# Performance work log

Measured on AMD Instinct MI355X. Metric: run time of the kernel, lower is better.

Reference implementation:

```python
import jax, jax.numpy as jnp
import numpy as np


def _conv2d(x, w, b):
    # NCHW valid conv, kernel shape OIHW
    y = jax.lax.conv_general_dilated(x, w, (1, 1), 'VALID',
                                     dimension_numbers=('NCHW', 'OIHW', 'NCHW'))
    return y + b[None, :, None, None]


def _rgcn(x, src, dst, edge_type, root, rel, bias):
    # PyG RGCNConv: out_i = x_i @ root + bias + sum_r mean_{j in N_r(i)} x_j @ W_r
    # x: [B, N, F]; src/dst: [E]; rel: [R, F, F]
    out = x @ root + bias
    N = x.shape[1]
    for r in range(rel.shape[0]):  # small fixed relation count
        m = (edge_type == r).astype(x.dtype)                # [E]
        msg = (x @ rel[r])[:, src] * m[None, :, None]       # [B, E, F]
        agg = jnp.zeros_like(out).at[:, dst].add(msg)       # [B, N, F]
        cnt = jnp.zeros((N,), x.dtype).at[dst].add(m)       # per-node relation degree
        out = out + agg / jnp.clip(cnt, 1.0)[None, :, None]
    return out


def setup_inputs() -> dict:
    key = jax.random.key(0)
    ks = jax.random.split(key, 16)
    B, C, N, T = 16, 3, 3000, 50
    E, R, S, F = 96000, 3, 500, 43  # F = 2*20 + 3
    observation = jax.random.normal(ks[0], (B, C, N, T), jnp.float32)
    last_action = jax.random.uniform(ks[1], (B, S + 1), dtype=jnp.float32)
    edge_index = jax.random.randint(ks[2], (2, E), 0, N, jnp.int32)
    edge_type = jax.random.randint(ks[3], (E,), 0, R, jnp.int32)
    nodes_to_select = jnp.sort(jax.random.randint(ks[4], (S,), 0, N, jnp.int32))

    def w(k, shape, fan_in):
        return jax.random.normal(k, shape, jnp.float32) / np.sqrt(fan_in).astype(np.float32)

    params = dict(
        ws1=w(ks[5], (3, 3, 1, 3), 9), bs1=jnp.zeros(3, jnp.float32),
        ws2=w(ks[6], (20, 3, 1, 48), 144), bs2=jnp.zeros(20, jnp.float32),
        wm1=w(ks[7], (3, 3, 1, 21), 63), bm1=jnp.zeros(3, jnp.float32),
        wm2=w(ks[8], (20, 3, 1, 30), 90), bm2=jnp.zeros(20, jnp.float32),
        root1=w(ks[9], (F, F), F), rel1=w(ks[10], (R, F, F), F), bias1=jnp.zeros(F, jnp.float32),
        root2=w(ks[11], (F, F), F), rel2=w(ks[12], (R, F, F), F), bias2=jnp.zeros(F, jnp.float32),
        wf=w(ks[13], (1, 87, 1, 1), 87), bf=jnp.zeros(1, jnp.float32),
    )
    return {"observation": observation, "last_action": last_action,
            "edge_index": edge_index, "edge_type": edge_type,
            "nodes_to_select": nodes_to_select, **params}


def reference(observation, last_action, edge_index, edge_type, nodes_to_select,
              ws1, bs1, ws2, bs2, wm1, bm1, wm2, bm2,
              root1, rel1, bias1, root2, rel2, bias2, wf, bf):
    relu = jax.nn.relu
    B = observation.shape[0]
    last_stocks = last_action[:, 1:][:, None, :, None]                      # [B,1,S,1]
    short = relu(_conv2d(relu(_conv2d(observation, ws1, bs1)), ws2, bs2))   # [B,20,N,1]
    mid = relu(_conv2d(relu(_conv2d(observation, wm1, bm1)), wm2, bm2))     # [B,20,N,1]
    longf = relu(jnp.max(observation, axis=3, keepdims=True))               # [B,3,N,1]
    temporal = jnp.concatenate([short, mid, longf], axis=1)                 # [B,43,N,1]
    x = jnp.transpose(temporal[..., 0], (0, 2, 1))                          # [B,N,43]
    src, dst = edge_index[0], edge_index[1]
    h = jax.nn.leaky_relu(_rgcn(x, src, dst, edge_type, root1, rel1, bias1), 0.01)
    h = jax.nn.leaky_relu(_rgcn(h, src, dst, edge_type, root2, rel2, bias2), 0.01)
    graph_features = jnp.transpose(h, (0, 2, 1))[..., None]                 # [B,43,N,1]
    feats = jnp.concatenate([temporal, graph_features], axis=1)             # [B,86,N,1]
    feats = feats[:, :, nodes_to_select, :]                                 # [B,86,S,1]
    feats = jnp.concatenate([last_stocks, feats], axis=1)                   # [B,87,S,1]
    out = _conv2d(feats, wf, bf)                                            # [B,1,S,1]
    cash = jnp.zeros((B, 1, 1, 1), out.dtype)  # cash bias zeroed in mu()
    logits = jnp.concatenate([cash, out], axis=2)[:, 0, :, 0]               # [B,S+1]
    return jax.nn.softmax(logits, axis=-1)  # softmax_temperature = 1
```

## Files before the change

kernel.cpp:

```cpp
#include <hip/hip_runtime.h>
#include <math.h>

#define NB 16
#define NC 3
#define NN 3000
#define NT 50
#define NE 96000
#define NR 3
#define NS 500
#define NF 43
#define NFP 44
#define NBF (NB*NFP)
#define NBKT (NR*NN)
#define CAP 96
#define PREF 24

#define XT_OFF   0
#define H1_OFF   (XT_OFF + NN*NBF)
#define LG_OFF   (H1_OFF + NN*NBF)
#define INT_BASE (LG_OFF + NB*(NS+1))
#define CNT_OFF  0
#define EBUF_OFF (CNT_OFF + NBKT)

#define TS 51

__global__ __launch_bounds__(256, 3) void k_front(
    const float* __restrict__ obs,
    const float* __restrict__ ws1, const float* __restrict__ bs1,
    const float* __restrict__ ws2, const float* __restrict__ bs2,
    const float* __restrict__ wm1, const float* __restrict__ bm1,
    const float* __restrict__ wm2, const float* __restrict__ bm2,
    float* __restrict__ x,
    const int* __restrict__ ei, const int* __restrict__ et,
    int* __restrict__ cnt, int* __restrict__ ebuf)
{
    __shared__ float smem[3 * 64 * TS];
    int tid = threadIdx.x;

    if (blockIdx.x >= 1500) {
        int e = (blockIdx.x - 1500) * 256 + tid;
        int bkt = et[e] * NN + ei[NE + e];
        int pos = atomicAdd(&cnt[bkt], 1);
        if (pos < CAP) ebuf[bkt * CAP + pos] = ei[e];
        return;
    }

    int wave = __builtin_amdgcn_readfirstlane(tid >> 6);
    int lane = tid & 63;
    bool isA = blockIdx.x < 750;
    int idx0 = (isA ? blockIdx.x : blockIdx.x - 750) * 64;

    #pragma unroll
    for (int k = 0; k < 19; ++k) {
        int f2 = k * 256 + tid;
        if (f2 < 4800) {
            int c = f2 / 1600;
            int rem = f2 - c * 1600;
            int nr = rem / 25;
            int tp = rem - nr * 25;
            int idx = idx0 + nr;
            int b = idx / NN, n = idx - b * NN;
            float2 u = *(const float2*)(obs + ((size_t)(b * NC + c) * NN + n) * NT + 2 * tp);
            float* d = &smem[(c * 64 + nr) * TS + 2 * tp];
            d[0] = u.x; d[1] = u.y;
        }
    }
    __syncthreads();

    #define SP(w, nd, o) smem[((w) * 64 + (nd)) * 23 + (o)]

    if (isA) {
        int base = 12 * wave;
        float wS[3][14];
        #pragma unroll
        for (int c = 0; c < 3; ++c) {
            const float* sr = &smem[(c * 64 + lane) * TS + base];
            #pragma unroll
            for (int jj = 0; jj < 14; ++jj) wS[c][jj] = sr[jj];
        }
        __syncthreads();

        float acc[20];
        #pragma unroll
        for (int o = 0; o < 20; ++o) acc[o] = 0.f;
        #pragma unroll
        for (int j = 0; j < 12; ++j) {
            float y[3];
            #pragma unroll
            for (int c = 0; c < 3; ++c) {
                float s = bs1[c];
                #pragma unroll
                for (int i = 0; i < 3; ++i)
                    #pragma unroll
                    for (int k = 0; k < 3; ++k)
                        s = fmaf(wS[i][j + k], ws1[(c * 3 + i) * 3 + k], s);
                y[c] = fmaxf(s, 0.f);
            }
            int gt = base + j;
            #pragma unroll
            for (int o = 0; o < 20; ++o) {
                float a = acc[o];
                #pragma unroll
                for (int c = 0; c < 3; ++c)
                    a = fmaf(y[c], ws2[(o * 3 + c) * 48 + gt], a);
                acc[o] = a;
            }
        }
        #pragma unroll
        for (int o = 0; o < 20; ++o) SP(wave, lane, o) = acc[o];
        __syncthreads();
        #pragma unroll
        for (int q = 0; q < 5; ++q) {
            int item = q * 256 + tid;
            int node = item / 20, o = item - node * 20;
            int g = idx0 + node;
            int bb = g / NN, nn = g - bb * NN;
            float s = ((SP(0, node, o) + SP(1, node, o)) +
                       (SP(2, node, o) + SP(3, node, o))) + bs2[o];
            x[(size_t)nn * NBF + bb * NFP + o] = fmaxf(s, 0.f);
        }
        return;
    }

    {
        int mbase = (wave < 3) ? 8 * wave : 24;
        int nld   = (wave < 3) ? 28 : 26;

        float s[3][8];
        #pragma unroll
        for (int c = 0; c < 3; ++c)
            #pragma unroll
            for (int t = 0; t < 8; ++t) s[c][t] = bm1[c];
        float cmax[3];
        float wA[28], wB[28];

        #define LOADW(buf, ch)                                              \
        {                                                                   \
            const float* sr = &smem[((ch) * 64 + lane) * TS + mbase];       \
            _Pragma("unroll")                                               \
            for (int t = 0; t < 28; ++t)                                    \
                buf[t] = (t < nld) ? sr[t] : 0.f;                           \
        }
        #define COMPW(buf, ii)                                              \
        {                                                                   \
            float m = buf[0];                                               \
            _Pragma("unroll")                                               \
            for (int t = 1; t < 28; ++t) m = fmaxf(m, buf[t]);              \
            cmax[ii] = m;                                                   \
            _Pragma("unroll")                                               \
            for (int c = 0; c < 3; ++c)                                     \
                _Pragma("unroll")                                           \
                for (int t = 0; t < 8; ++t) {                               \
                    float a = s[c][t];                                      \
                    _Pragma("unroll")                                       \
                    for (int k = 0; k < 21; ++k)                            \
                        a = fmaf(buf[t + k], wm1[(c * 3 + (ii)) * 21 + k], a); \
                    s[c][t] = a;                                            \
                }                                                           \
        }

        LOADW(wA, 0)
        LOADW(wB, 1)
        COMPW(wA, 0)
        LOADW(wA, 2)
        COMPW(wB, 1)
        COMPW(wA, 2)
        #undef LOADW
        #undef COMPW
        __syncthreads();

        float acc[20];
        #pragma unroll
        for (int o = 0; o < 20; ++o) acc[o] = 0.f;
        int cntM = (wave < 3) ? 8 : 6;
        #pragma unroll
        for (int j = 0; j < 8; ++j) {
            if (j < cntM) {
                float y0 = fmaxf(s[0][j], 0.f);
                float y1 = fmaxf(s[1][j], 0.f);
                float y2 = fmaxf(s[2][j], 0.f);
                int gt = mbase + j;
                #pragma unroll
                for (int o = 0; o < 20; ++o) {
                    float a = acc[o];
                    a = fmaf(y0, wm2[(o * 3 + 0) * 30 + gt], a);
                    a = fmaf(y1, wm2[(o * 3 + 1) * 30 + gt], a);
                    a = fmaf(y2, wm2[(o * 3 + 2) * 30 + gt], a);
                    acc[o] = a;
                }
            }
        }
        #pragma unroll
        for (int o = 0; o < 20; ++o) SP(wave, lane, o) = acc[o];
        #pragma unroll
        for (int c = 0; c < 3; ++c) SP(wave, lane, 20 + c) = cmax[c];
    }
    __syncthreads();
    #pragma unroll
    for (int q = 0; q < 6; ++q) {
        int item = q * 256 + tid;
        if (item < 1472) {
            int node = item / 23, o = item - node * 23;
            int g = idx0 + node;
            int bb = g / NN, nn = g - bb * NN;
            size_t row = (size_t)nn * NBF + bb * NFP;
            if (o < 20) {
                float s = ((SP(0, node, o) + SP(1, node, o)) +
                           (SP(2, node, o) + SP(3, node, o))) + bm2[o];
                x[row + 20 + o] = fmaxf(s, 0.f);
            } else {
                float m = fmaxf(fmaxf(SP(0, node, o), SP(1, node, o)),
                                fmaxf(SP(2, node, o), SP(3, node, o)));
                x[row + 40 + (o - 20)] = fmaxf(m, 0.f);
            }
        }
    }
    #undef SP
}

template<bool LEAKY, bool SEL>
__global__ __launch_bounds__(256) void k_rgcn(
    const float* __restrict__ in, const float* __restrict__ xsrc,
    const int* __restrict__ cnt, const int* __restrict__ ebuf,
    const int* __restrict__ sel,
    const float* __restrict__ root, const float* __restrict__ rel,
    const float* __restrict__ bias,
    const float* __restrict__ la, const float* __restrict__ wf,
    const float* __restrict__ bf,
    float* __restrict__ out)
{
    __shared__ __align__(16) float lrow[4][NBF];
    __shared__ float sP[8][4][NFP];

    int tid = threadIdx.x;
    int wave = __builtin_amdgcn_readfirstlane(tid >> 6);
    int lane = tid & 63;
    int i = blockIdx.x;
    int node = __builtin_amdgcn_readfirstlane(SEL ? sel[i] : i);

    const float* wbase = (wave == 0) ? root : (rel + (size_t)(wave - 1) * NF * NF);
    float wsl[43];
    #pragma unroll
    for (int j = 0; j < 43; ++j)
        wsl[j] = (lane < NF) ? wbase[j * NF + lane] : 0.f;

    if (wave == 3) {
        const float4* p4 = (const float4*)(in + (size_t)node * NBF);
        #pragma unroll
        for (int k = 0; k < 3; ++k) {
            int fi = k * 64 + lane;
            if (fi < 176) {
                float4 v = p4[fi];
                if (LEAKY) {
                    v.x = v.x >= 0.f ? v.x : 0.01f * v.x;
                    v.y = v.y >= 0.f ? v.y : 0.01f * v.y;
                    v.z = v.z >= 0.f ? v.z : 0.01f * v.z;
                    v.w = v.w >= 0.f ? v.w : 0.01f * v.w;
                }
                *(float4*)&lrow[0][4 * fi] = v;
            }
        }
    } else {
        int bkt = wave * NN + node;
        int cvr = __builtin_amdgcn_readfirstlane(cnt[bkt]);
        float ic = 1.0f / fmaxf((float)cvr, 1.0f);
        int cv = cvr > CAP ? CAP : cvr;
        const int* eb = ebuf + (size_t)bkt * CAP;

        int id[PREF];
        #pragma unroll
        for (int k = 0; k < PREF / 4; ++k) {
            int4 q = *(const int4*)(eb + 4 * k);
            id[4 * k + 0] = __builtin_amdgcn_readfirstlane(q.x);
            id[4 * k + 1] = __builtin_amdgcn_readfirstlane(q.y);
            id[4 * k + 2] = __builtin_amdgcn_readfirstlane(q.z);
            id[4 * k + 3] = __builtin_amdgcn_readfirstlane(q.w);
        }

        float4 a0 = {0.f, 0.f, 0.f, 0.f};
        float4 a1 = {0.f, 0.f, 0.f, 0.f};
        float4 a2 = {0.f, 0.f, 0.f, 0.f};

        #define GATHER(PTR)                                                  \
        {                                                                    \
            const float4* p = (const float4*)(PTR);                          \
            float4 v0 = p[lane];                                             \
            float4 v1 = p[64 + lane];                                        \
            if (LEAKY) {                                                     \
                v0.x = v0.x >= 0.f ? v0.x : 0.01f * v0.x;                    \
                v0.y = v0.y >= 0.f ? v0.y : 0.01f * v0.y;                    \
                v0.z = v0.z >= 0.f ? v0.z : 0.01f * v0.z;                    \
                v0.w = v0.w >= 0.f ? v0.w : 0.01f * v0.w;                    \
                v1.x = v1.x >= 0.f ? v1.x : 0.01f * v1.x;                    \
                v1.y = v1.y >= 0.f ? v1.y : 0.01f * v1.y;                    \
                v1.z = v1.z >= 0.f ? v1.z : 0.01f * v1.z;                    \
                v1.w = v1.w >= 0.f ? v1.w : 0.01f * v1.w;                    \
            }                                                                \
            a0.x += v0.x; a0.y += v0.y; a0.z += v0.z; a0.w += v0.w;          \
            a1.x += v1.x; a1.y += v1.y; a1.z += v1.z; a1.w += v1.w;          \
            if (lane < 48) {                                                 \
                float4 v2 = p[128 + lane];                                   \
                if (LEAKY) {                                                 \
                    v2.x = v2.x >= 0.f ? v2.x : 0.01f * v2.x;                \
                    v2.y = v2.y >= 0.f ? v2.y : 0.01f * v2.y;                \
                    v2.z = v2.z >= 0.f ? v2.z : 0.01f * v2.z;                \
                    v2.w = v2.w >= 0.f ? v2.w : 0.01f * v2.w;                \
                }                                                            \
                a2.x += v2.x; a2.y += v2.y; a2.z += v2.z; a2.w += v2.w;      \
            }                                                                \
        }

        #pragma unroll
        for (int e = 0; e < PREF; ++e) {
            if (e < cv) GATHER(in + (size_t)id[e] * NBF)
        }
        for (int e = PREF; e < cv; ++e) {
            int i0 = __builtin_amdgcn_readfirstlane(eb[e]);
            GATHER(in + (size_t)i0 * NBF)
        }
        #undef GATHER

        float* dst = &lrow[wave + 1][0];
        a0.x *= ic; a0.y *= ic; a0.z *= ic; a0.w *= ic;
        a1.x *= ic; a1.y *= ic; a1.z *= ic; a1.w *= ic;
        *(float4*)&dst[4 * lane] = a0;
        *(float4*)&dst[4 * (64 + lane)] = a1;
        if (lane < 48) {
            a2.x *= ic; a2.y *= ic; a2.z *= ic; a2.w *= ic;
            *(float4*)&dst[4 * (128 + lane)] = a2;
        }
    }
    __syncthreads();

    for (int h = 0; h < 2; ++h) {
        #pragma unroll
        for (int rr = 0; rr < 8; ++rr) {
            int b = h * 8 + rr;
            const float4* a4 = (const float4*)&lrow[wave][b * NFP];
            float a0 = 0.f, a1 = 0.f, a2 = 0.f, a3 = 0.f;
            #pragma unroll
            for (int c = 0; c < 10; ++c) {
                float4 v = a4[c];
                a0 = fmaf(v.x, wsl[4 * c], a0);
                a1 = fmaf(v.y, wsl[4 * c + 1], a1);
                a2 = fmaf(v.z, wsl[4 * c + 2], a2);
                a3 = fmaf(v.w, wsl[4 * c + 3], a3);
            }
            {
                float4 v = a4[10];
                a0 = fmaf(v.x, wsl[40], a0);
                a1 = fmaf(v.y, wsl[41], a1);
                a2 = fmaf(v.z, wsl[42], a2);
            }
            if (lane < NF) sP[rr][wave][lane] = (a0 + a1) + (a2 + a3);
        }
        __syncthreads();

        int r0 = 2 * wave, r1 = 2 * wave + 1;
        int b0 = h * 8 + r0, b1 = h * 8 + r1;
        if (!SEL) {
            if (lane < NF) {
                float bi_ = bias[lane];
                float s0 = ((sP[r0][0][lane] + sP[r0][1][lane]) +
                            (sP[r0][2][lane] + sP[r0][3][lane])) + bi_;
                float s1 = ((sP[r1][0][lane] + sP[r1][1][lane]) +
                            (sP[r1][2][lane] + sP[r1][3][lane])) + bi_;
                out[(size_t)i * NBF + b0 * NFP + lane] = s0;
                out[(size_t)i * NBF + b1 * NFP + lane] = s1;
            }
        } else {
            float p0 = 0.f, p1 = 0.f;
            if (lane < NF) {
                float bi_ = bias[lane];
                float s0 = ((sP[r0][0][lane] + sP[r0][1][lane]) +
                            (sP[r0][2][lane] + sP[r0][3][lane])) + bi_;
                float s1 = ((sP[r1][0][lane] + sP[r1][1][lane]) +
                            (sP[r1][2][lane] + sP[r1][3][lane])) + bi_;
                s0 = s0 >= 0.f ? s0 : 0.01f * s0;
                s1 = s1 >= 0.f ? s1 : 0.01f * s1;
                float x0 = xsrc[(size_t)node * NBF + b0 * NFP + lane];
                float x1 = xsrc[(size_t)node * NBF + b1 * NFP + lane];
                p0 = fmaf(wf[44 + lane], s0, wf[1 + lane] * x0);
                p1 = fmaf(wf[44 + lane], s1, wf[1 + lane] * x1);
            }
            #pragma unroll
            for (int o = 32; o > 0; o >>= 1) {
                p0 += __shfl_down(p0, o);
                p1 += __shfl_down(p1, o);
            }
            if (lane == 0) {
                out[(size_t)b0 * (NS + 1) + 1 + i] =
                    p0 + bf[0] + wf[0] * la[b0 * (NS + 1) + 1 + i];
                out[(size_t)b1 * (NS + 1) + 1 + i] =
                    p1 + bf[0] + wf[0] * la[b1 * (NS + 1) + 1 + i];
            }
        }
        __syncthreads();
    }
}

__device__ inline float wred_max(float v) {
    #pragma unroll
    for (int o = 32; o > 0; o >>= 1) v = fmaxf(v, __shfl_down(v, o));
    return v;
}
__device__ inline float wred_sum(float v) {
    #pragma unroll
    for (int o = 32; o > 0; o >>= 1) v += __shfl_down(v, o);
    return v;
}

__global__ __launch_bounds__(512) void k_softmax(
    const float* __restrict__ lg, float* __restrict__ out)
{
    __shared__ float sred[8];
    __shared__ float sbc[2];
    int b = blockIdx.x, tid = threadIdx.x;

    float val = -3.0e38f;
    if (tid <= NS) val = (tid == 0) ? 0.f : lg[(size_t)b * (NS + 1) + tid];

    float m = wred_max(val);
    if ((tid & 63) == 0) sred[tid >> 6] = m;
    __syncthreads();
    if (tid == 0) {
        float mm = sred[0];
        #pragma unroll
        for (int i = 1; i < 8; ++i) mm = fmaxf(mm, sred[i]);
        sbc[0] = mm;
    }
    __syncthreads();
    float mx = sbc[0];
    float e = (tid <= NS) ? expf(val - mx) : 0.f;
    float s = wred_sum(e);
    if ((tid & 63) == 0) sred[tid >> 6] = s;
    __syncthreads();
    if (tid == 0) {
        float t = 0.f;
        #pragma unroll
        for (int i = 0; i < 8; ++i) t += sred[i];
        sbc[1] = t;
    }
    __syncthreads();
    if (tid <= NS) out[(size_t)b * (NS + 1) + tid] = e / sbc[1];
}

extern "C" void kernel_launch(void* const* d_in, const int* in_sizes, int n_in,
                              void* d_out, int out_size, void* d_ws, size_t ws_size,
                              hipStream_t stream)
{
    const float* obs   = (const float*)d_in[0];
    const float* la    = (const float*)d_in[1];
    const int*   ei    = (const int*)d_in[2];
    const int*   et    = (const int*)d_in[3];
    const int*   nodes = (const int*)d_in[4];
    const float* ws1 = (const float*)d_in[5],  *bs1 = (const float*)d_in[6];
    const float* ws2 = (const float*)d_in[7],  *bs2 = (const float*)d_in[8];
    const float* wm1 = (const float*)d_in[9],  *bm1 = (const float*)d_in[10];
    const float* wm2 = (const float*)d_in[11], *bm2 = (const float*)d_in[12];
    const float* root1 = (const float*)d_in[13], *rel1 = (const float*)d_in[14], *bias1 = (const float*)d_in[15];
    const float* root2 = (const float*)d_in[16], *rel2 = (const float*)d_in[17], *bias2 = (const float*)d_in[18];
    const float* wf = (const float*)d_in[19], *bf = (const float*)d_in[20];

    float* wsp = (float*)d_ws;
    float* x   = wsp + XT_OFF;
    float* h1  = wsp + H1_OFF;
    float* lg  = wsp + LG_OFF;
    int*   ibase = (int*)(wsp + INT_BASE);
    int*   cnt   = ibase + CNT_OFF;
    int*   ebuf  = ibase + EBUF_OFF;

    hipMemsetAsync(cnt, 0, NBKT * sizeof(int), stream);

    k_front<<<1875, 256, 0, stream>>>(
        obs, ws1, bs1, ws2, bs2, wm1, bm1, wm2, bm2, x, ei, et, cnt, ebuf);

    k_rgcn<false, false><<<NN, 256, 0, stream>>>(
        x, nullptr, cnt, ebuf, nullptr, root1, rel1, bias1,
        nullptr, nullptr, nullptr, h1);

    k_rgcn<true, true><<<NS, 256, 0, stream>>>(
        h1, x, cnt, ebuf, nodes, root2, rel2, bias2,
        la, wf, bf, lg);

    k_softmax<<<NB, 512, 0, stream>>>(lg, (float*)d_out);
}
```

Before: 217.1 us.

## Merge short and mid temporal conv blocks so each observation tile loads once

```diff
diff --git a/kernel.cpp b/kernel.cpp
--- a/kernel.cpp
+++ b/kernel.cpp
@@ -37,8 +37,8 @@
     __shared__ float smem[3 * 64 * TS];
     int tid = threadIdx.x;
 
-    if (blockIdx.x >= 1500) {
-        int e = (blockIdx.x - 1500) * 256 + tid;
+    if (blockIdx.x >= 750) {
+        int e = (blockIdx.x - 750) * 256 + tid;
         int bkt = et[e] * NN + ei[NE + e];
         int pos = atomicAdd(&cnt[bkt], 1);
         if (pos < CAP) ebuf[bkt * CAP + pos] = ei[e];
@@ -47,8 +47,7 @@
 
     int wave = __builtin_amdgcn_readfirstlane(tid >> 6);
     int lane = tid & 63;
-    bool isA = blockIdx.x < 750;
-    int idx0 = (isA ? blockIdx.x : blockIdx.x - 750) * 64;
+    int idx0 = blockIdx.x * 64;
 
     #pragma unroll
     for (int k = 0; k < 19; ++k) {
@@ -67,71 +66,16 @@
     }
     __syncthreads();
 
-    #define SP(w, nd, o) smem[((w) * 64 + (nd)) * 23 + (o)]
-
-    if (isA) {
-        int base = 12 * wave;
-        float wS[3][14];
-        #pragma unroll
-        for (int c = 0; c < 3; ++c) {
-            const float* sr = &smem[(c * 64 + lane) * TS + base];
-            #pragma unroll
-            for (int jj = 0; jj < 14; ++jj) wS[c][jj] = sr[jj];
-        }
-        __syncthreads();
-
-        float acc[20];
-        #pragma unroll
-        for (int o = 0; o < 20; ++o) acc[o] = 0.f;
-        #pragma unroll
-        for (int j = 0; j < 12; ++j) {
-            float y[3];
-            #pragma unroll
-            for (int c = 0; c < 3; ++c) {
-                float s = bs1[c];
-                #pragma unroll
-                for (int i = 0; i < 3; ++i)
-                    #pragma unroll
-                    for (int k = 0; k < 3; ++k)
-                        s = fmaf(wS[i][j + k], ws1[(c * 3 + i) * 3 + k], s);
-                y[c] = fmaxf(s, 0.f);
-            }
-            int gt = base + j;
-            #pragma unroll
-            for (int o = 0; o < 20; ++o) {
-                float a = acc[o];
-                #pragma unroll
-                for (int c = 0; c < 3; ++c)
-                    a = fmaf(y[c], ws2[(o * 3 + c) * 48 + gt], a);
-                acc[o] = a;
-            }
-        }
-        #pragma unroll
-        for (int o = 0; o < 20; ++o) SP(wave, lane, o) = acc[o];
-        __syncthreads();
-        #pragma unroll
-        for (int q = 0; q < 5; ++q) {
-            int item = q * 256 + tid;
-            int node = item / 20, o = item - node * 20;
-            int g = idx0 + node;
-            int bb = g / NN, nn = g - bb * NN;
-            float s = ((SP(0, node, o) + SP(1, node, o)) +
-                       (SP(2, node, o) + SP(3, node, o))) + bs2[o];
-            x[(size_t)nn * NBF + bb * NFP + o] = fmaxf(s, 0.f);
-        }
-        return;
-    }
-
+    int mbase = (wave < 3) ? 8 * wave : 24;
+    int nld   = (wave < 3) ? 28 : 26;
+
+    float s[3][8];
+    #pragma unroll
+    for (int c = 0; c < 3; ++c)
+        #pragma unroll
+        for (int t = 0; t < 8; ++t) s[c][t] = bm1[c];
+    float cmax[3];
     {
-        int mbase = (wave < 3) ? 8 * wave : 24;
-        int nld   = (wave < 3) ? 28 : 26;
-
-        float s[3][8];
-        #pragma unroll
-        for (int c = 0; c < 3; ++c)
-            #pragma unroll
-            for (int t = 0; t < 8; ++t) s[c][t] = bm1[c];
-        float cmax[3];
         float wA[28], wB[28];
 
         #define LOADW(buf, ch)                                              \
@@ -167,11 +111,12 @@
         COMPW(wA, 2)
         #undef LOADW
         #undef COMPW
-        __syncthreads();
-
-        float acc[20];
-        #pragma unroll
-        for (int o = 0; o < 20; ++o) acc[o] = 0.f;
+    }
+
+    float accB[20];
+    #pragma unroll
+    for (int o = 0; o < 20; ++o) accB[o] = 0.f;
+    {
         int cntM = (wave < 3) ? 8 : 6;
         #pragma unroll
         for (int j = 0; j < 8; ++j) {
@@ -182,19 +127,32 @@
                 int gt = mbase + j;
                 #pragma unroll
                 for (int o = 0; o < 20; ++o) {
-                    float a = acc[o];
+                    float a = accB[o];
                     a = fmaf(y0, wm2[(o * 3 + 0) * 30 + gt], a);
                     a = fmaf(y1, wm2[(o * 3 + 1) * 30 + gt], a);
                     a = fmaf(y2, wm2[(o * 3 + 2) * 30 + gt], a);
-                    acc[o] = a;
+                    accB[o] = a;
                 }
             }
         }
-        #pragma unroll
-        for (int o = 0; o < 20; ++o) SP(wave, lane, o) = acc[o];
-        #pragma unroll
-        for (int c = 0; c < 3; ++c) SP(wave, lane, 20 + c) = cmax[c];
-    }
+    }
+
+    int base = 12 * wave;
+    float wS[3][14];
+    #pragma unroll
+    for (int c = 0; c < 3; ++c) {
+        const float* sr = &smem[(c * 64 + lane) * TS + base];
+        #pragma unroll
+        for (int jj = 0; jj < 14; ++jj) wS[c][jj] = sr[jj];
+    }
+    __syncthreads();
+
+    #define SP(w, nd, o) smem[((w) * 64 + (nd)) * 23 + (o)]
+
+    #pragma unroll
+    for (int o = 0; o < 20; ++o) SP(wave, lane, o) = accB[o];
+    #pragma unroll
+    for (int c = 0; c < 3; ++c) SP(wave, lane, 20 + c) = cmax[c];
     __syncthreads();
     #pragma unroll
     for (int q = 0; q < 6; ++q) {
@@ -205,15 +163,58 @@
             int bb = g / NN, nn = g - bb * NN;
             size_t row = (size_t)nn * NBF + bb * NFP;
             if (o < 20) {
-                float s = ((SP(0, node, o) + SP(1, node, o)) +
+                float v = ((SP(0, node, o) + SP(1, node, o)) +
                            (SP(2, node, o) + SP(3, node, o))) + bm2[o];
-                x[row + 20 + o] = fmaxf(s, 0.f);
+                x[row + 20 + o] = fmaxf(v, 0.f);
             } else {
                 float m = fmaxf(fmaxf(SP(0, node, o), SP(1, node, o)),
                                 fmaxf(SP(2, node, o), SP(3, node, o)));
                 x[row + 40 + (o - 20)] = fmaxf(m, 0.f);
             }
         }
+    }
+    __syncthreads();
+
+    {
+        float acc[20];
+        #pragma unroll
+        for (int o = 0; o < 20; ++o) acc[o] = 0.f;
+        #pragma unroll
+        for (int j = 0; j < 12; ++j) {
+            float y[3];
+            #pragma unroll
+            for (int c = 0; c < 3; ++c) {
+                float v = bs1[c];
+                #pragma unroll
+                for (int i = 0; i < 3; ++i)
+                    #pragma unroll
+                    for (int k = 0; k < 3; ++k)
+                        v = fmaf(wS[i][j + k], ws1[(c * 3 + i) * 3 + k], v);
+                y[c] = fmaxf(v, 0.f);
+            }
+            int gt = base + j;
+            #pragma unroll
+            for (int o = 0; o < 20; ++o) {
+                float a = acc[o];
+                #pragma unroll
+                for (int c = 0; c < 3; ++c)
+                    a = fmaf(y[c], ws2[(o * 3 + c) * 48 + gt], a);
+                acc[o] = a;
+            }
+        }
+        #pragma unroll
+        for (int o = 0; o < 20; ++o) SP(wave, lane, o) = acc[o];
+    }
+    __syncthreads();
+    #pragma unroll
+    for (int q = 0; q < 5; ++q) {
+        int item = q * 256 + tid;
+        int node = item / 20, o = item - node * 20;
+        int g = idx0 + node;
+        int bb = g / NN, nn = g - bb * NN;
+        float v = ((SP(0, node, o) + SP(1, node, o)) +
+                   (SP(2, node, o) + SP(3, node, o))) + bs2[o];
+        x[(size_t)nn * NBF + bb * NFP + o] = fmaxf(v, 0.f);
     }
     #undef SP
 }
@@ -472,7 +473,7 @@
 
     hipMemsetAsync(cnt, 0, NBKT * sizeof(int), stream);
 
-    k_front<<<1875, 256, 0, stream>>>(
+    k_front<<<1125, 256, 0, stream>>>(
         obs, ws1, bs1, ws2, bs2, wm1, bm1, wm2, bm2, x, ei, et, cnt, ebuf);
 
     k_rgcn<false, false><<<NN, 256, 0, stream>>>(
```

Result: no change. 217.8 us (+0.3%).
